# Optimization experiments

Measured on AMD Instinct MI355X. Metric: run time of the kernel, lower is better.

Reference implementation:

```python
import jax, jax.numpy as jnp
import numpy as np

EPS = 1e-12
PERP_EPS = 1e-10


def setup_inputs() -> dict:
    key = jax.random.key(0)
    k1, k2, k3 = jax.random.split(key, 3)
    B, D, H, W = 32, 64, 32, 32
    K = 1024
    inputs = jax.random.normal(k1, (B, D, H, W), dtype=jnp.float32)
    codebooks = jax.random.normal(k2, (K, D), dtype=jnp.float32)
    noise = jax.random.normal(k3, (B * H * W, D), dtype=jnp.float32)
    return {"inputs": inputs, "codebooks": codebooks, "noise": noise}


def reference(inputs, codebooks, noise):
    B, D, H, W = inputs.shape
    K = codebooks.shape[0]
    # NCHW -> NHWC -> (N, D)
    x = jnp.transpose(inputs, (0, 2, 3, 1)).reshape(-1, D)
    distances = (
        jnp.sum(x * x, axis=1, keepdims=True)
        - 2.0 * jnp.einsum("nd,kd->nk", x, codebooks)
        + jnp.sum(codebooks * codebooks, axis=1)[None, :]
    )
    min_indices = jnp.argmin(distances, axis=1)  # (N,)
    best_entries = codebooks[min_indices]  # gather, (N, D)
    # per-row norm-matched noise injection (NSVQ)
    norm_best = jnp.sqrt(jnp.sum((x - best_entries) ** 2, axis=1, keepdims=True))
    norm_rand = jnp.sqrt(jnp.sum(noise * noise, axis=1, keepdims=True))
    vq_error = (norm_best / norm_rand + EPS) * noise
    quantized = x + vq_error
    quantized = jnp.transpose(quantized.reshape(B, H, W, D), (0, 3, 1, 2))
    # perplexity from one-hot usage histogram
    N = x.shape[0]
    counts = jnp.zeros((K,), dtype=jnp.float32).at[min_indices].add(1.0)
    avg_probs = counts / N
    perplexity = jnp.exp(-jnp.sum(avg_probs * jnp.log(avg_probs + PERP_EPS)))
    return quantized, perplexity
```

## Files before the change

### kernel.cpp

```cpp
#include <hip/hip_runtime.h>
#include <hip/hip_bf16.h>
#include <math.h>

#define BB 32
#define DD 64
#define HH 32
#define WW 32
#define NN (BB * HH * WW)
#define KK 1024
#define HW (HH * WW)
#define NQ (BB * DD * HH * WW)
#define NBLK 512

#define EPS_F 1e-12f
#define PERP_EPS_F 1e-10f
#define DIST_BIAS 512.0f

typedef __attribute__((ext_vector_type(8))) __bf16 bf16x8;
typedef __attribute__((ext_vector_type(8))) unsigned short u16x8;
typedef __attribute__((ext_vector_type(4))) float f32x4;

static __device__ __forceinline__ unsigned short f2bf(float f) {
    union { float f; unsigned int u; } c;
    c.f = f;
    unsigned int r = c.u + 0x7FFFu + ((c.u >> 16) & 1u);
    return (unsigned short)(r >> 16);
}

__global__ __launch_bounds__(256) void k_prep(const float* __restrict__ cb,
                                              unsigned short* __restrict__ cbs,
                                              float* __restrict__ cnorm,
                                              unsigned int* __restrict__ counts) {
    const int gt = blockIdx.x * 256 + threadIdx.x;
    const int j = gt >> 2;
    const int q = gt & 3;
    const int jt = j >> 4;
    const int col = j & 15;
    const float4* src = reinterpret_cast<const float4*>(cb + (size_t)j * DD + q * 16);
    float4 v0 = src[0], v1 = src[1], v2 = src[2], v3 = src[3];
    float s = v0.x * v0.x + v0.y * v0.y + v0.z * v0.z + v0.w * v0.w
            + v1.x * v1.x + v1.y * v1.y + v1.z * v1.z + v1.w * v1.w
            + v2.x * v2.x + v2.y * v2.y + v2.z * v2.z + v2.w * v2.w
            + v3.x * v3.x + v3.y * v3.y + v3.z * v3.z + v3.w * v3.w;

#pragma unroll
    for (int i2 = 0; i2 < 2; ++i2) {
        const int quad_lin = q * 2 + i2;
        const int frag = quad_lin >> 2;
        const int quad = quad_lin & 3;
        const int lane = quad * 16 + col;
        u16x8 pk;
        if (i2 == 0) {
            pk[0] = f2bf(v0.x); pk[1] = f2bf(v0.y); pk[2] = f2bf(v0.z); pk[3] = f2bf(v0.w);
            pk[4] = f2bf(v1.x); pk[5] = f2bf(v1.y); pk[6] = f2bf(v1.z); pk[7] = f2bf(v1.w);
        } else {
            pk[0] = f2bf(v2.x); pk[1] = f2bf(v2.y); pk[2] = f2bf(v2.z); pk[3] = f2bf(v2.w);
            pk[4] = f2bf(v3.x); pk[5] = f2bf(v3.y); pk[6] = f2bf(v3.z); pk[7] = f2bf(v3.w);
        }
        *reinterpret_cast<u16x8*>(cbs + ((size_t)(jt * 2 + frag) * 64 + lane) * 8) = pk;
    }

    s += __shfl_xor(s, 1);
    s += __shfl_xor(s, 2);
    if (q == 0) {
        cnorm[j] = s + DIST_BIAS;
        counts[j] = 0u;
    }
}

__global__ __launch_bounds__(512) void k_main(const float* __restrict__ inp,
                                              const unsigned short* __restrict__ cbs,
                                              const float* __restrict__ cb,
                                              const float* __restrict__ cnorm,
                                              const float* __restrict__ noise,
                                              unsigned int* __restrict__ counts,
                                              float* __restrict__ out) {
    __shared__ float xs[64 * 65];
    __shared__ __align__(16) unsigned short scratch[64 * 72];
    __shared__ unsigned int mg[64 * 4];
    __shared__ int jwin[64];
    __shared__ float sscale[64];

    unsigned short* xls = scratch;
    unsigned short* nsu = scratch;

    const int tid = threadIdx.x;
    const int nbase = blockIdx.x * 64;
    const int b = nbase >> 10;
    const int hwbase = nbase & 1023;
    const float* xg = inp + (size_t)b * (DD * HW) + hwbase;

    const int lane = tid & 63;
    const int wid = tid >> 6;
    const int w = wid & 3;
    const int rh = wid >> 2;
    const int rbase = rh * 32;
    const int col = lane & 15;
    const int quad = lane >> 4;

#pragma unroll
    for (int i = 0; i < 8; ++i) {
        int idx = i * 512 + tid;
        int d = idx >> 6, r = idx & 63;
        xs[d * 65 + r] = xg[d * HW + r];
    }
    __syncthreads();

    {
        const int rr = tid >> 3;
        const int sg = tid & 7;
        u16x8 pk;
#pragma unroll
        for (int j2 = 0; j2 < 8; ++j2)
            pk[j2] = f2bf(xs[(sg * 8 + j2) * 65 + rr]);
        *reinterpret_cast<u16x8*>(&xls[rr * 72 + sg * 8]) = pk;
    }
    __syncthreads();

    const bf16x8 a00 = *reinterpret_cast<const bf16x8*>(&xls[(rbase + col) * 72 + quad * 8]);
    const bf16x8 a01 = *reinterpret_cast<const bf16x8*>(&xls[(rbase + col) * 72 + 32 + quad * 8]);
    const bf16x8 a10 = *reinterpret_cast<const bf16x8*>(&xls[(rbase + 16 + col) * 72 + quad * 8]);
    const bf16x8 a11 = *reinterpret_cast<const bf16x8*>(&xls[(rbase + 16 + col) * 72 + 32 + quad * 8]);

    unsigned int minu[8];
#pragma unroll
    for (int s = 0; s < 8; ++s) minu[s] = 0xFFFFFFFFu;

    const unsigned short* bp = cbs + (size_t)w * 16 * 1024 + lane * 8;
    const float* cnp = cnorm + w * 256 + col;

    bf16x8 bb[2][4];
#pragma unroll
    for (int pg = 0; pg < 2; ++pg) {
#pragma unroll
        for (int t2 = 0; t2 < 2; ++t2) {
            const size_t off = (size_t)(pg * 2 + t2) * 1024;
            bb[pg][t2 * 2]     = *reinterpret_cast<const bf16x8*>(bp + off);
            bb[pg][t2 * 2 + 1] = *reinterpret_cast<const bf16x8*>(bp + off + 512);
        }
    }

#pragma unroll
    for (int g = 0; g < 8; ++g) {
        const int cb_ = g & 1;
#pragma unroll
        for (int t2 = 0; t2 < 2; ++t2) {
            const int jt = g * 2 + t2;
            f32x4 acc0 = {0.f, 0.f, 0.f, 0.f};
            f32x4 acc1 = {0.f, 0.f, 0.f, 0.f};
            acc0 = __builtin_amdgcn_mfma_f32_16x16x32_bf16(a00, bb[cb_][t2 * 2], acc0, 0, 0, 0);
            acc0 = __builtin_amdgcn_mfma_f32_16x16x32_bf16(a01, bb[cb_][t2 * 2 + 1], acc0, 0, 0, 0);
            acc1 = __builtin_amdgcn_mfma_f32_16x16x32_bf16(a10, bb[cb_][t2 * 2], acc1, 0, 0, 0);
            acc1 = __builtin_amdgcn_mfma_f32_16x16x32_bf16(a11, bb[cb_][t2 * 2 + 1], acc1, 0, 0, 0);
            const float cnt = cnp[jt * 16];
            const unsigned int jc = (unsigned int)(jt * 16 + col);
#pragma unroll
            for (int r = 0; r < 4; ++r) {
                float d0 = fmaf(-2.0f, acc0[r], cnt);
                unsigned int u0 = (__float_as_uint(d0) & ~255u) | jc;
                minu[r] = minu[r] < u0 ? minu[r] : u0;
                float d1 = fmaf(-2.0f, acc1[r], cnt);
                unsigned int u1 = (__float_as_uint(d1) & ~255u) | jc;
                minu[4 + r] = minu[4 + r] < u1 ? minu[4 + r] : u1;
            }
        }
        if (g < 6) {
#pragma unroll
            for (int t2 = 0; t2 < 2; ++t2) {
                const size_t off = (size_t)((g + 2) * 2 + t2) * 1024;
                bb[cb_][t2 * 2]     = *reinterpret_cast<const bf16x8*>(bp + off);
                bb[cb_][t2 * 2 + 1] = *reinterpret_cast<const bf16x8*>(bp + off + 512);
            }
        }
    }

#pragma unroll
    for (int s = 0; s < 8; ++s) {
        unsigned int v = minu[s];
#pragma unroll
        for (int off = 1; off < 16; off <<= 1) {
            unsigned int ov = (unsigned int)__shfl_xor((int)v, off);
            v = v < ov ? v : ov;
        }
        if (col == 0) {
            const int rloc = rbase + (s >> 2) * 16 + quad * 4 + (s & 3);
            mg[rloc * 4 + w] = v;
        }
    }
    __syncthreads();

    if (tid < 64) {
        unsigned int best = mg[tid * 4 + 0];
        unsigned int bestd = best & ~255u;
        int j = (int)(best & 255u);
#pragma unroll
        for (int q = 1; q < 4; ++q) {
            unsigned int uq = mg[tid * 4 + q];
            unsigned int dq = uq & ~255u;
            if (dq < bestd) { bestd = dq; j = q * 256 + (int)(uq & 255u); }
        }
        jwin[tid] = j;
        atomicAdd(&counts[j], 1u);
    }
    __syncthreads();

    {
        const int rr2 = tid >> 3;
        const int ql = tid & 7;
        const int j = jwin[rr2];
        const float* cr = cb + (size_t)j * DD + ql * 8;
        const float4 c0 = *reinterpret_cast<const float4*>(cr);
        const float4 c1 = *reinterpret_cast<const float4*>(cr + 4);
        const float* nr = noise + (size_t)(nbase + rr2) * DD + ql * 8;
        const float4 nz0 = *reinterpret_cast<const float4*>(nr);
        const float4 nz1 = *reinterpret_cast<const float4*>(nr + 4);
        float sb = 0.0f, sn = 0.0f, df;
        df = xs[(ql * 8 + 0) * 65 + rr2] - c0.x; sb = fmaf(df, df, sb); sn = fmaf(nz0.x, nz0.x, sn);
        df = xs[(ql * 8 + 1) * 65 + rr2] - c0.y; sb = fmaf(df, df, sb); sn = fmaf(nz0.y, nz0.y, sn);
        df = xs[(ql * 8 + 2) * 65 + rr2] - c0.z; sb = fmaf(df, df, sb); sn = fmaf(nz0.z, nz0.z, sn);
        df = xs[(ql * 8 + 3) * 65 + rr2] - c0.w; sb = fmaf(df, df, sb); sn = fmaf(nz0.w, nz0.w, sn);
        df = xs[(ql * 8 + 4) * 65 + rr2] - c1.x; sb = fmaf(df, df, sb); sn = fmaf(nz1.x, nz1.x, sn);
        df = xs[(ql * 8 + 5) * 65 + rr2] - c1.y; sb = fmaf(df, df, sb); sn = fmaf(nz1.y, nz1.y, sn);
        df = xs[(ql * 8 + 6) * 65 + rr2] - c1.z; sb = fmaf(df, df, sb); sn = fmaf(nz1.z, nz1.z, sn);
        df = xs[(ql * 8 + 7) * 65 + rr2] - c1.w; sb = fmaf(df, df, sb); sn = fmaf(nz1.w, nz1.w, sn);
        sb += __shfl_xor(sb, 1); sb += __shfl_xor(sb, 2); sb += __shfl_xor(sb, 4);
        sn += __shfl_xor(sn, 1); sn += __shfl_xor(sn, 2); sn += __shfl_xor(sn, 4);
        if (ql == 0) sscale[rr2] = sqrtf(sb) / sqrtf(sn) + EPS_F;
        u16x8 pk;
        pk[0] = f2bf(nz0.x); pk[1] = f2bf(nz0.y); pk[2] = f2bf(nz0.z); pk[3] = f2bf(nz0.w);
        pk[4] = f2bf(nz1.x); pk[5] = f2bf(nz1.y); pk[6] = f2bf(nz1.z); pk[7] = f2bf(nz1.w);
        *reinterpret_cast<u16x8*>(&nsu[rr2 * 65 + ql * 8]) = pk;
    }
    __syncthreads();

#pragma unroll
    for (int i = 0; i < 8; ++i) {
        int idx = i * 512 + tid;
        int d = idx >> 6, r = idx & 63;
        unsigned int nu = (unsigned int)nsu[r * 65 + d] << 16;
        out[(size_t)(b * DD + d) * HW + hwbase + r] =
            xs[d * 65 + r] + sscale[r] * __uint_as_float(nu);
    }
}

__global__ __launch_bounds__(1024) void k_perp(const unsigned int* __restrict__ counts,
                                               float* __restrict__ out) {
    __shared__ float red[16];
    const int tid = threadIdx.x;
    const int lane = tid & 63;
    float p = (float)counts[tid] * (1.0f / (float)NN);
    float t = p * logf(p + PERP_EPS_F);
#pragma unroll
    for (int off = 32; off > 0; off >>= 1) t += __shfl_down(t, off);
    if (lane == 0) red[tid >> 6] = t;
    __syncthreads();
    if (tid == 0) {
        float s = 0.0f;
#pragma unroll
        for (int i = 0; i < 16; ++i) s += red[i];
        out[0] = expf(-s);
    }
}

extern "C" void kernel_launch(void* const* d_in, const int* in_sizes, int n_in,
                              void* d_out, int out_size, void* d_ws, size_t ws_size,
                              hipStream_t stream) {
    (void)in_sizes; (void)n_in; (void)out_size; (void)ws_size;
    const float* inp   = (const float*)d_in[0];
    const float* cb    = (const float*)d_in[1];
    const float* noise = (const float*)d_in[2];
    float* out = (float*)d_out;

    char* ws = (char*)d_ws;
    float*          cnorm  = (float*)ws;
    unsigned int*   counts = (unsigned int*)(ws + 4096);
    unsigned short* cbs    = (unsigned short*)(ws + 8192);

    k_prep<<<16, 256, 0, stream>>>(cb, cbs, cnorm, counts);
    k_main<<<NBLK, 512, 0, stream>>>(inp, cbs, cb, cnorm, noise, counts, out);
    k_perp<<<1, 1024, 0, stream>>>(counts, out + NQ);
}
```

Before: 94.49 us.

## Derive best-code residual norm from argmin distance and prefetch noise and codebook early

Instead of gathering the winning fp32 codebook row and recomputing ||x-c||^2, the kernel reconstructs it from the packed minimum distance (bf16 GEMM result minus bias) plus a precomputed ||x||^2. Noise loads and the bf16 codebook fragment loads are hoisted ahead of the first barrier so their latency overlaps the input staging. This removes a dependent global gather after the argmin reduction. The trade-off is that the residual norm now comes from the bf16-approximated, low-bit-truncated distance, which can be less accurate and may go slightly negative, hence the clamp at zero.

```diff
diff --git a/kernel.cpp b/kernel.cpp
--- a/kernel.cpp
+++ b/kernel.cpp
@@ -70,7 +70,6 @@
 
 __global__ __launch_bounds__(512) void k_main(const float* __restrict__ inp,
                                               const unsigned short* __restrict__ cbs,
-                                              const float* __restrict__ cb,
                                               const float* __restrict__ cnorm,
                                               const float* __restrict__ noise,
                                               unsigned int* __restrict__ counts,
@@ -78,7 +77,8 @@
     __shared__ float xs[64 * 65];
     __shared__ __align__(16) unsigned short scratch[64 * 72];
     __shared__ unsigned int mg[64 * 4];
-    __shared__ int jwin[64];
+    __shared__ float dw[64];
+    __shared__ float sxs[64];
     __shared__ float sscale[64];
 
     unsigned short* xls = scratch;
@@ -98,22 +98,47 @@
     const int col = lane & 15;
     const int quad = lane >> 4;
 
+    const unsigned short* bp = cbs + (size_t)w * 16 * 1024 + lane * 8;
+    const float* cnp = cnorm + w * 256 + col;
+
+    bf16x8 bb[2][4];
+#pragma unroll
+    for (int pg = 0; pg < 2; ++pg) {
+#pragma unroll
+        for (int t2 = 0; t2 < 2; ++t2) {
+            const size_t off = (size_t)(pg * 2 + t2) * 1024;
+            bb[pg][t2 * 2]     = *reinterpret_cast<const bf16x8*>(bp + off);
+            bb[pg][t2 * 2 + 1] = *reinterpret_cast<const bf16x8*>(bp + off + 512);
+        }
+    }
+
 #pragma unroll
     for (int i = 0; i < 8; ++i) {
         int idx = i * 512 + tid;
         int d = idx >> 6, r = idx & 63;
         xs[d * 65 + r] = xg[d * HW + r];
     }
+
+    const int rrn = tid >> 3;
+    const int qln = tid & 7;
+    const float* nr = noise + (size_t)(nbase + rrn) * DD + qln * 8;
+    const float4 nz0 = *reinterpret_cast<const float4*>(nr);
+    const float4 nz1 = *reinterpret_cast<const float4*>(nr + 4);
+
     __syncthreads();
 
     {
-        const int rr = tid >> 3;
-        const int sg = tid & 7;
         u16x8 pk;
-#pragma unroll
-        for (int j2 = 0; j2 < 8; ++j2)
-            pk[j2] = f2bf(xs[(sg * 8 + j2) * 65 + rr]);
-        *reinterpret_cast<u16x8*>(&xls[rr * 72 + sg * 8]) = pk;
+        float sx = 0.0f;
+#pragma unroll
+        for (int j2 = 0; j2 < 8; ++j2) {
+            float v = xs[(qln * 8 + j2) * 65 + rrn];
+            pk[j2] = f2bf(v);
+            sx = fmaf(v, v, sx);
+        }
+        *reinterpret_cast<u16x8*>(&xls[rrn * 72 + qln * 8]) = pk;
+        sx += __shfl_xor(sx, 1); sx += __shfl_xor(sx, 2); sx += __shfl_xor(sx, 4);
+        if (qln == 0) sxs[rrn] = sx;
     }
     __syncthreads();
 
@@ -125,20 +150,6 @@
     unsigned int minu[8];
 #pragma unroll
     for (int s = 0; s < 8; ++s) minu[s] = 0xFFFFFFFFu;
-
-    const unsigned short* bp = cbs + (size_t)w * 16 * 1024 + lane * 8;
-    const float* cnp = cnorm + w * 256 + col;
-
-    bf16x8 bb[2][4];
-#pragma unroll
-    for (int pg = 0; pg < 2; ++pg) {
-#pragma unroll
-        for (int t2 = 0; t2 < 2; ++t2) {
-            const size_t off = (size_t)(pg * 2 + t2) * 1024;
-            bb[pg][t2 * 2]     = *reinterpret_cast<const bf16x8*>(bp + off);
-            bb[pg][t2 * 2 + 1] = *reinterpret_cast<const bf16x8*>(bp + off + 512);
-        }
-    }
 
 #pragma unroll
     for (int g = 0; g < 8; ++g) {
@@ -199,37 +210,26 @@
             unsigned int dq = uq & ~255u;
             if (dq < bestd) { bestd = dq; j = q * 256 + (int)(uq & 255u); }
         }
-        jwin[tid] = j;
+        dw[tid] = __uint_as_float(bestd) - DIST_BIAS;
         atomicAdd(&counts[j], 1u);
     }
     __syncthreads();
 
     {
-        const int rr2 = tid >> 3;
-        const int ql = tid & 7;
-        const int j = jwin[rr2];
-        const float* cr = cb + (size_t)j * DD + ql * 8;
-        const float4 c0 = *reinterpret_cast<const float4*>(cr);
-        const float4 c1 = *reinterpret_cast<const float4*>(cr + 4);
-        const float* nr = noise + (size_t)(nbase + rr2) * DD + ql * 8;
-        const float4 nz0 = *reinterpret_cast<const float4*>(nr);
-        const float4 nz1 = *reinterpret_cast<const float4*>(nr + 4);
-        float sb = 0.0f, sn = 0.0f, df;
-        df = xs[(ql * 8 + 0) * 65 + rr2] - c0.x; sb = fmaf(df, df, sb); sn = fmaf(nz0.x, nz0.x, sn);
-        df = xs[(ql * 8 + 1) * 65 + rr2] - c0.y; sb = fmaf(df, df, sb); sn = fmaf(nz0.y, nz0.y, sn);
-        df = xs[(ql * 8 + 2) * 65 + rr2] - c0.z; sb = fmaf(df, df, sb); sn = fmaf(nz0.z, nz0.z, sn);
-        df = xs[(ql * 8 + 3) * 65 + rr2] - c0.w; sb = fmaf(df, df, sb); sn = fmaf(nz0.w, nz0.w, sn);
-        df = xs[(ql * 8 + 4) * 65 + rr2] - c1.x; sb = fmaf(df, df, sb); sn = fmaf(nz1.x, nz1.x, sn);
-        df = xs[(ql * 8 + 5) * 65 + rr2] - c1.y; sb = fmaf(df, df, sb); sn = fmaf(nz1.y, nz1.y, sn);
-        df = xs[(ql * 8 + 6) * 65 + rr2] - c1.z; sb = fmaf(df, df, sb); sn = fmaf(nz1.z, nz1.z, sn);
-        df = xs[(ql * 8 + 7) * 65 + rr2] - c1.w; sb = fmaf(df, df, sb); sn = fmaf(nz1.w, nz1.w, sn);
-        sb += __shfl_xor(sb, 1); sb += __shfl_xor(sb, 2); sb += __shfl_xor(sb, 4);
+        float sn = 0.0f;
+        sn = fmaf(nz0.x, nz0.x, sn); sn = fmaf(nz0.y, nz0.y, sn);
+        sn = fmaf(nz0.z, nz0.z, sn); sn = fmaf(nz0.w, nz0.w, sn);
+        sn = fmaf(nz1.x, nz1.x, sn); sn = fmaf(nz1.y, nz1.y, sn);
+        sn = fmaf(nz1.z, nz1.z, sn); sn = fmaf(nz1.w, nz1.w, sn);
         sn += __shfl_xor(sn, 1); sn += __shfl_xor(sn, 2); sn += __shfl_xor(sn, 4);
-        if (ql == 0) sscale[rr2] = sqrtf(sb) / sqrtf(sn) + EPS_F;
+        if (qln == 0) {
+            float nb2 = fmaxf(dw[rrn] + sxs[rrn], 0.0f);
+            sscale[rrn] = sqrtf(nb2) / sqrtf(sn) + EPS_F;
+        }
         u16x8 pk;
         pk[0] = f2bf(nz0.x); pk[1] = f2bf(nz0.y); pk[2] = f2bf(nz0.z); pk[3] = f2bf(nz0.w);
         pk[4] = f2bf(nz1.x); pk[5] = f2bf(nz1.y); pk[6] = f2bf(nz1.z); pk[7] = f2bf(nz1.w);
-        *reinterpret_cast<u16x8*>(&nsu[rr2 * 65 + ql * 8]) = pk;
+        *reinterpret_cast<u16x8*>(&nsu[rrn * 65 + qln * 8]) = pk;
     }
     __syncthreads();
 
@@ -277,6 +277,6 @@
     unsigned short* cbs    = (unsigned short*)(ws + 8192);
 
     k_prep<<<16, 256, 0, stream>>>(cb, cbs, cnorm, counts);
-    k_main<<<NBLK, 512, 0, stream>>>(inp, cbs, cb, cnorm, noise, counts, out);
+    k_main<<<NBLK, 512, 0, stream>>>(inp, cbs, cnorm, noise, counts, out);
     k_perp<<<1, 1024, 0, stream>>>(counts, out + NQ);
 }
```

New measurement: 92.43 us (median of 2 runs). 2.2% less time.
